# Performance work log

Measured on AMD Instinct MI355X. Metric: run time of the kernel, lower is better.

The kernel has to match this reference:

```python
import jax, jax.numpy as jnp
import numpy as np

K = 7      # involution kernel size
G = 16     # groups
EPS = 1e-5 # BatchNorm eps (torch default)


def setup_inputs() -> dict:
    key = jax.random.key(0)
    ks = jax.random.split(key, 5)
    N, C, H, W = 4, 256, 56, 56
    Cr = C // 4            # ratio=4 reduction channels
    KKG = K * K * G        # 784 dynamic-kernel channels
    x = jax.random.normal(ks[0], (N, C, H, W), dtype=jnp.float32)
    w1 = jax.random.normal(ks[1], (Cr, C), dtype=jnp.float32) * 0.05
    b1 = jax.random.normal(ks[2], (Cr,), dtype=jnp.float32) * 0.05
    gamma = jnp.ones((Cr,), dtype=jnp.float32)
    beta = jnp.zeros((Cr,), dtype=jnp.float32)
    mean = jnp.zeros((Cr,), dtype=jnp.float32)
    var = jnp.ones((Cr,), dtype=jnp.float32)
    w2 = jax.random.normal(ks[3], (KKG, Cr), dtype=jnp.float32) * 0.05
    b2 = jax.random.normal(ks[4], (KKG,), dtype=jnp.float32) * 0.05
    return {"x": x, "w1": w1, "b1": b1, "gamma": gamma, "beta": beta,
            "mean": mean, "var": var, "w2": w2, "b2": b2}


def _involution(x, w1, b1, gamma, beta, mean, var, w2, b2):
    N, C, H, W = x.shape
    pad = K // 2
    # --- kernel-generating branch (stride=1 => AvgPool is identity) ---
    t = jnp.einsum('nchw,oc->nohw', x, w1) + b1[None, :, None, None]   # 1x1 conv
    inv_std = jax.lax.rsqrt(var + EPS)
    t = (t - mean[None, :, None, None]) * (inv_std * gamma)[None, :, None, None] \
        + beta[None, :, None, None]                                    # BatchNorm (inference)
    t = jax.nn.relu(t)
    ker = jnp.einsum('nohw,ko->nkhw', t, w2) + b2[None, :, None, None] # (N, K*K*G, H, W)
    ker = ker.reshape(N, G, K * K, H, W)                               # per-group dyn kernels
    # --- unfold (im2col), torch layout: (N, C, K*K, H, W), kk = kh*K + kw ---
    xp = jnp.pad(x, ((0, 0), (0, 0), (pad, pad), (pad, pad)))
    patches = jnp.stack(
        [xp[:, :, i:i + H, j:j + W] for i in range(K) for j in range(K)], axis=2)
    patches = patches.reshape(N, G, C // G, K * K, H, W)
    # --- per-pixel weighted sum over kernel positions ---
    out = jnp.einsum('ngckhw,ngkhw->ngchw', patches, ker)
    return out.reshape(N, C, H, W)


def reference(x, w1, b1, gamma, beta, mean, var, w2, b2):
    return _involution(x, w1, b1, gamma, beta, mean, var, w2, b2)
```

## Files before the change

kernel.cpp:

```cpp
#include <hip/hip_runtime.h>


namespace {
constexpr int Nn  = 4;
constexpr int Cc  = 256;
constexpr int Hh  = 56;
constexpr int Ww  = 56;
constexpr int HW  = Hh * Ww;
constexpr int NPX = Nn * HW;
constexpr int KK  = 49;
}

extern "C" __global__ void __launch_bounds__(256, 4)
k1_conv_bn_relu(const float* __restrict__ x,  const float* __restrict__ w1,
                const float* __restrict__ b1, const float* __restrict__ gamma,
                const float* __restrict__ beta, const float* __restrict__ mean,
                const float* __restrict__ var,  float* __restrict__ t)
{
    const int lane = threadIdx.x & 63;
    const int wv   = threadIdx.x >> 6;
    const int px   = blockIdx.x * 64 + lane;
    const int o0   = __builtin_amdgcn_readfirstlane((int)blockIdx.y * 32 + wv * 8);

    const int n  = px / HW;
    const int hw = px - n * HW;
    const float* xb = x + (size_t)n * Cc * HW + hw;

    float acc[8];
#pragma unroll
    for (int i = 0; i < 8; ++i) acc[i] = 0.f;

#pragma unroll 4
    for (int c = 0; c < Cc; ++c) {
        const float xv = xb[(size_t)c * HW];
#pragma unroll
        for (int oo = 0; oo < 8; ++oo)
            acc[oo] = fmaf(xv, w1[(o0 + oo) * Cc + c], acc[oo]);
    }

#pragma unroll
    for (int oo = 0; oo < 8; ++oo) {
        const int o = o0 + oo;
        const float inv = rsqrtf(var[o] + 1e-5f);
        const float sc  = gamma[o] * inv;
        const float sh  = fmaf(b1[o] - mean[o], sc, beta[o]);
        float v = fmaf(acc[oo], sc, sh);
        t[(size_t)o * NPX + px] = v > 0.f ? v : 0.f;
    }
}

extern "C" __global__ void __launch_bounds__(256, 2)
k2_involution(const float* __restrict__ x,  const float* __restrict__ t,
              const float* __restrict__ w2, const float* __restrict__ b2,
              float* __restrict__ out)
{
    const int lane = threadIdx.x & 63;
    const int wv   = threadIdx.x >> 6;
    const int nh   = blockIdx.x;
    const int n    = nh / Hh;
    const int h    = nh - n * Hh;
    const int g    = __builtin_amdgcn_readfirstlane((int)blockIdx.y * 4 + wv);
    const int wcl  = lane < Ww ? lane : (Ww - 1);
    const int pxb  = nh * Ww;

    float treg[64];
#pragma unroll
    for (int o = 0; o < 64; ++o)
        treg[o] = t[o * NPX + pxb + wcl];

    float acc[16];
#pragma unroll
    for (int i = 0; i < 16; ++i) acc[i] = 0.f;

    const float* xg  = x  + (size_t)n * Cc * HW + (size_t)(g * 16) * HW;
    const float* w2g = w2 + g * KK * 64;
    const float* b2g = b2 + g * KK;

    for (int kh = 0; kh < 7; ++kh) {
        const int hh = h + kh - 3;
        if (hh < 0 || hh >= Hh) continue;
        const float* xrow = xg + hh * Ww;
#pragma unroll
        for (int kw = 0; kw < 7; ++kw) {
            const int k = kh * 7 + kw;
            const float* w2row = w2g + k * 64;
            float p0 = 0.f, p1 = 0.f, p2 = 0.f, p3 = 0.f;
#pragma unroll
            for (int o = 0; o < 64; o += 4) {
                p0 = fmaf(treg[o + 0], w2row[o + 0], p0);
                p1 = fmaf(treg[o + 1], w2row[o + 1], p1);
                p2 = fmaf(treg[o + 2], w2row[o + 2], p2);
                p3 = fmaf(treg[o + 3], w2row[o + 3], p3);
            }
            const float kerk = ((p0 + p1) + (p2 + p3)) + b2g[k];
            const int ww = lane + kw - 3;
            if (ww >= 0 && ww < Ww) {
#pragma unroll
                for (int c = 0; c < 16; ++c)
                    acc[c] = fmaf(xrow[(size_t)c * HW + ww], kerk, acc[c]);
            }
        }
    }

    if (lane < Ww) {
        float* og = out + (size_t)n * Cc * HW + (size_t)(g * 16) * HW + h * Ww + lane;
#pragma unroll
        for (int c = 0; c < 16; ++c)
            og[c * HW] = acc[c];
    }
}

extern "C" void kernel_launch(void* const* d_in, const int* in_sizes, int n_in,
                              void* d_out, int out_size, void* d_ws, size_t ws_size,
                              hipStream_t stream)
{
    const float* x     = (const float*)d_in[0];
    const float* w1    = (const float*)d_in[1];
    const float* b1    = (const float*)d_in[2];
    const float* gamma = (const float*)d_in[3];
    const float* beta  = (const float*)d_in[4];
    const float* mean  = (const float*)d_in[5];
    const float* var   = (const float*)d_in[6];
    const float* w2    = (const float*)d_in[7];
    const float* b2    = (const float*)d_in[8];

    float* t   = (float*)d_ws;
    float* out = (float*)d_out;

    k1_conv_bn_relu<<<dim3(NPX / 64, 2), 256, 0, stream>>>(
        x, w1, b1, gamma, beta, mean, var, t);
    k2_involution<<<dim3(Nn * Hh, 4), 256, 0, stream>>>(
        x, t, w2, b2, out);
}
```

Measured before the change: 88.84 us.

## Split involution kernel positions across waves with LDS reduction; shrink conv outputs per wave

The involution kernel now assigns one group per block and spreads the 49 kernel positions across the 4 waves, reducing the partial channel sums through shared memory. The grid grows from 4 to 16 blocks in y and occupancy hints rise. The 1x1 conv kernel computes 4 output channels per wave instead of 8, doubling the grid to expose more parallelism. The cost is redundant reads of x/t per block, extra LDS traffic and a barrier, plus more t reloads in the conv stage.

New measurement: 83.37 us. 6.2% less time.

```diff
diff --git a/kernel.cpp b/kernel.cpp
--- a/kernel.cpp
+++ b/kernel.cpp
@@ -11,55 +11,57 @@
 constexpr int KK  = 49;
 }
 
-extern "C" __global__ void __launch_bounds__(256, 4)
+extern "C" __global__ void __launch_bounds__(256, 8)
 k1_conv_bn_relu(const float* __restrict__ x,  const float* __restrict__ w1,
                 const float* __restrict__ b1, const float* __restrict__ gamma,
                 const float* __restrict__ beta, const float* __restrict__ mean,
                 const float* __restrict__ var,  float* __restrict__ t)
 {
     const int lane = threadIdx.x & 63;
-    const int wv   = threadIdx.x >> 6;
+    const int wv   = __builtin_amdgcn_readfirstlane(threadIdx.x >> 6);
     const int px   = blockIdx.x * 64 + lane;
-    const int o0   = __builtin_amdgcn_readfirstlane((int)blockIdx.y * 32 + wv * 8);
+    const int o0   = __builtin_amdgcn_readfirstlane(((int)blockIdx.y * 4 + wv) * 4);
 
     const int n  = px / HW;
     const int hw = px - n * HW;
     const float* xb = x + (size_t)n * Cc * HW + hw;
 
-    float acc[8];
-#pragma unroll
-    for (int i = 0; i < 8; ++i) acc[i] = 0.f;
+    float a0 = 0.f, a1 = 0.f, a2 = 0.f, a3 = 0.f;
 
-#pragma unroll 4
+#pragma unroll 8
     for (int c = 0; c < Cc; ++c) {
         const float xv = xb[(size_t)c * HW];
-#pragma unroll
-        for (int oo = 0; oo < 8; ++oo)
-            acc[oo] = fmaf(xv, w1[(o0 + oo) * Cc + c], acc[oo]);
+        a0 = fmaf(xv, w1[(o0 + 0) * Cc + c], a0);
+        a1 = fmaf(xv, w1[(o0 + 1) * Cc + c], a1);
+        a2 = fmaf(xv, w1[(o0 + 2) * Cc + c], a2);
+        a3 = fmaf(xv, w1[(o0 + 3) * Cc + c], a3);
     }
 
+    float accs[4] = {a0, a1, a2, a3};
 #pragma unroll
-    for (int oo = 0; oo < 8; ++oo) {
+    for (int oo = 0; oo < 4; ++oo) {
         const int o = o0 + oo;
         const float inv = rsqrtf(var[o] + 1e-5f);
         const float sc  = gamma[o] * inv;
         const float sh  = fmaf(b1[o] - mean[o], sc, beta[o]);
-        float v = fmaf(acc[oo], sc, sh);
+        float v = fmaf(accs[oo], sc, sh);
         t[(size_t)o * NPX + px] = v > 0.f ? v : 0.f;
     }
 }
 
-extern "C" __global__ void __launch_bounds__(256, 2)
+extern "C" __global__ void __launch_bounds__(256, 4)
 k2_involution(const float* __restrict__ x,  const float* __restrict__ t,
               const float* __restrict__ w2, const float* __restrict__ b2,
               float* __restrict__ out)
 {
+    __shared__ float red[4][16][64];
+
     const int lane = threadIdx.x & 63;
-    const int wv   = threadIdx.x >> 6;
+    const int wv   = __builtin_amdgcn_readfirstlane(threadIdx.x >> 6);
     const int nh   = blockIdx.x;
     const int n    = nh / Hh;
     const int h    = nh - n * Hh;
-    const int g    = __builtin_amdgcn_readfirstlane((int)blockIdx.y * 4 + wv);
+    const int g    = __builtin_amdgcn_readfirstlane((int)blockIdx.y);
     const int wcl  = lane < Ww ? lane : (Ww - 1);
     const int pxb  = nh * Ww;
 
@@ -67,6 +69,9 @@
 #pragma unroll
     for (int o = 0; o < 64; ++o)
         treg[o] = t[o * NPX + pxb + wcl];
+#pragma unroll
+    for (int o = 0; o < 64; ++o)
+        asm volatile("" : "+v"(treg[o]));
 
     float acc[16];
 #pragma unroll
@@ -76,37 +81,44 @@
     const float* w2g = w2 + g * KK * 64;
     const float* b2g = b2 + g * KK;
 
-    for (int kh = 0; kh < 7; ++kh) {
+    for (int k = wv; k < KK; k += 4) {
+        const int kh = k / 7;
+        const int kw = k - kh * 7;
         const int hh = h + kh - 3;
         if (hh < 0 || hh >= Hh) continue;
-        const float* xrow = xg + hh * Ww;
+        const float* xrow  = xg + hh * Ww;
+        const float* w2row = w2g + k * 64;
+        float p0 = 0.f, p1 = 0.f, p2 = 0.f, p3 = 0.f;
 #pragma unroll
-        for (int kw = 0; kw < 7; ++kw) {
-            const int k = kh * 7 + kw;
-            const float* w2row = w2g + k * 64;
-            float p0 = 0.f, p1 = 0.f, p2 = 0.f, p3 = 0.f;
+        for (int o = 0; o < 64; o += 4) {
+            p0 = fmaf(treg[o + 0], w2row[o + 0], p0);
+            p1 = fmaf(treg[o + 1], w2row[o + 1], p1);
+            p2 = fmaf(treg[o + 2], w2row[o + 2], p2);
+            p3 = fmaf(treg[o + 3], w2row[o + 3], p3);
+        }
+        const float kerk = ((p0 + p1) + (p2 + p3)) + b2g[k];
+        const int ww = lane + kw - 3;
+        if (ww >= 0 && ww < Ww) {
 #pragma unroll
-            for (int o = 0; o < 64; o += 4) {
-                p0 = fmaf(treg[o + 0], w2row[o + 0], p0);
-                p1 = fmaf(treg[o + 1], w2row[o + 1], p1);
-                p2 = fmaf(treg[o + 2], w2row[o + 2], p2);
-                p3 = fmaf(treg[o + 3], w2row[o + 3], p3);
-            }
-            const float kerk = ((p0 + p1) + (p2 + p3)) + b2g[k];
-            const int ww = lane + kw - 3;
-            if (ww >= 0 && ww < Ww) {
-#pragma unroll
-                for (int c = 0; c < 16; ++c)
-                    acc[c] = fmaf(xrow[(size_t)c * HW + ww], kerk, acc[c]);
-            }
+            for (int c = 0; c < 16; ++c)
+                acc[c] = fmaf(xrow[(size_t)c * HW + ww], kerk, acc[c]);
         }
     }
+
+#pragma unroll
+    for (int c = 0; c < 16; ++c)
+        red[wv][c][lane] = acc[c];
+    __syncthreads();
 
     if (lane < Ww) {
         float* og = out + (size_t)n * Cc * HW + (size_t)(g * 16) * HW + h * Ww + lane;
 #pragma unroll
-        for (int c = 0; c < 16; ++c)
-            og[c * HW] = acc[c];
+        for (int j = 0; j < 4; ++j) {
+            const int c = wv * 4 + j;
+            const float s = red[0][c][lane] + red[1][c][lane]
+                          + red[2][c][lane] + red[3][c][lane];
+            og[c * HW] = s;
+        }
     }
 }
 
@@ -127,8 +139,8 @@
     float* t   = (float*)d_ws;
     float* out = (float*)d_out;
 
-    k1_conv_bn_relu<<<dim3(NPX / 64, 2), 256, 0, stream>>>(
+    k1_conv_bn_relu<<<dim3(NPX / 64, 4), 256, 0, stream>>>(
         x, w1, b1, gamma, beta, mean, var, t);
-    k2_involution<<<dim3(Nn * Hh, 4), 256, 0, stream>>>(
+    k2_involution<<<dim3(Nn * Hh, 16), 256, 0, stream>>>(
         x, t, w2, b2, out);
 }
```
